# Optimization experiments

Measured on AMD Instinct MI355X. Metric: run time of the kernel, lower is better.

Reference implementation:

```python
import jax, jax.numpy as jnp
import numpy as np

N_B, N_A = 32, 48
H_IN, E_IN, H_H, H_G, NCELLS = 64, 32, 64, 16, 5


def setup_inputs() -> dict:
    key = jax.random.key(0)
    ks = jax.random.split(key, 10)
    A = (jax.random.uniform(ks[0], (N_B, N_A, N_A)) < 0.3).astype(jnp.float32)
    h = jax.random.normal(ks[1], (N_B, N_A, H_IN), dtype=jnp.float32)
    E = jax.random.normal(ks[2], (N_B, N_A, N_A, E_IN), dtype=jnp.float32)
    s_h = 1.0 / np.sqrt(H_IN)
    s_e = 1.0 / np.sqrt(E_IN)
    s_g = 1.0 / np.sqrt(H_H)
    W_h = jax.random.uniform(ks[3], (H_IN, H_H), minval=-s_h, maxval=s_h)
    b_h = jax.random.uniform(ks[4], (H_H,), minval=-s_h, maxval=s_h)
    W_e = jax.random.uniform(ks[5], (E_IN, H_G * H_H), minval=-s_e, maxval=s_e)
    b_e = jax.random.uniform(ks[6], (H_G * H_H,), minval=-s_e, maxval=s_e)
    W_ih = jax.random.uniform(ks[7], (3 * H_H, H_G), minval=-s_g, maxval=s_g)
    W_hh = jax.random.uniform(ks[8], (3 * H_H, H_H), minval=-s_g, maxval=s_g)
    b_ih = jax.random.uniform(jax.random.fold_in(key, 11), (3 * H_H,), minval=-s_g, maxval=s_g)
    b_hh = jax.random.uniform(jax.random.fold_in(key, 12), (3 * H_H,), minval=-s_g, maxval=s_g)
    return {"A": A, "h": h, "E": E, "W_h": W_h, "b_h": b_h, "W_e": W_e, "b_e": b_e,
            "W_ih": W_ih, "b_ih": b_ih, "W_hh": W_hh, "b_hh": b_hh}


def _gru_cell(x, hprev, W_ih, b_ih, W_hh, b_hh):
    # PyTorch GRUCell semantics
    gi = x @ W_ih.T + b_ih      # [N, 3*H_H]
    gh = hprev @ W_hh.T + b_hh  # [N, 3*H_H]
    i_r, i_z, i_n = jnp.split(gi, 3, axis=-1)
    h_r, h_z, h_n = jnp.split(gh, 3, axis=-1)
    r = jax.nn.sigmoid(i_r + h_r)
    z = jax.nn.sigmoid(i_z + h_z)
    n = jnp.tanh(i_n + r * h_n)
    return (1.0 - z) * n + z * hprev


def reference(A, h, E, W_h, b_h, W_e, b_e, W_ih, b_ih, W_hh, b_hh):
    N_b, n_a = h.shape[0], A.shape[1]
    maskh = (jnp.sum(A, axis=-1, keepdims=True) > 0.1).astype(jnp.float32)  # [B,n,1]
    hv = jax.nn.relu(h @ W_h + b_h) * maskh                                 # [B,n,H_H]
    Ee = jax.nn.relu(E @ W_e + b_e).reshape(N_b, n_a, n_a, H_G, H_H)
    Ee = Ee * A[..., None, None]                                            # mask edges
    # E.matmul(h).sum(dim=1) == (sum_i E[b,i,j]) @ h[b,j]; precompute the i-sum
    Esum = Ee.sum(axis=1)                                                   # [B,j,G,H]
    hc = hv  # [B,n,H_H]
    for _ in range(NCELLS):
        M = jnp.einsum('bjgh,bjh->bjg', Esum, hc).reshape(N_b * n_a, H_G)
        hc = _gru_cell(M, hc.reshape(N_b * n_a, H_H), W_ih, b_ih, W_hh, b_hh)
        hc = hc.reshape(N_b, n_a, H_H)
    return hc
```

## Files before the change

### kernel.cpp

```cpp
#include <hip/hip_runtime.h>
#include <stdint.h>

#define NB 32
#define NA 48
#define HIN 64
#define EIN 32
#define HH 64
#define HG 16
#define NCELLS 5
#define GH 1024
#define EROW 40

typedef __attribute__((ext_vector_type(8))) short short8;
typedef __attribute__((ext_vector_type(4))) float float4v;

__device__ __forceinline__ unsigned short f2bf(float f) {
    union { float f; unsigned int u; } v; v.f = f;
    unsigned int u = v.u + 0x7FFF + ((v.u >> 16) & 1);
    return (unsigned short)(u >> 16);
}
__device__ __forceinline__ float bf2f(unsigned short s) {
    union { unsigned int u; float f; } v; v.u = ((unsigned int)s) << 16;
    return v.f;
}

__global__ __launch_bounds__(256) void swizzle_We(const float* __restrict__ W_e,
                                                  unsigned short* __restrict__ hiB,
                                                  unsigned short* __restrict__ loB) {
    const int o  = blockIdx.x * 256 + threadIdx.x;
    const int ct = o >> 9;
    const int l  = (o >> 3) & 63;
    const int jj = o & 7;
    const int k  = (l >> 4) * 8 + jj;
    const int c  = ct * 16 + (l & 15);
    const float x = W_e[k * GH + c];
    const unsigned short hb = f2bf(x);
    hiB[o] = hb;
    loB[o] = f2bf(x - bf2f(hb));
}

__global__ __launch_bounds__(256) void prep_gw(const float* __restrict__ W_ih,
                                               const float* __restrict__ W_hh,
                                               float4* __restrict__ gw4) {
    const int idx = blockIdx.x * 256 + threadIdx.x;
    if (idx >= 20 * 192) return;
    const int j = idx / 192;
    const int c = idx - j * 192;
    float4 v;
    if (j < 4)  v = *(const float4*)(W_ih + c * HG + 4 * j);
    else        v = *(const float4*)(W_hh + c * HH + 4 * (j - 4));
    gw4[idx] = v;
}

template <int NT>
__device__ __forceinline__ void edge_phase(
    const unsigned short* __restrict__ hiB, const unsigned short* __restrict__ loB,
    const float* __restrict__ b_e,
    const unsigned short* EcolH, const unsigned short* EcolL,
    const int* ilist, int cnt, int wave, int lane, int mrow, int quad,
    float* Esum_s)
{
    const float4v zero4 = {0.0f, 0.0f, 0.0f, 0.0f};
    short8 aH[NT ? NT : 1], aL[NT ? NT : 1];
    float4v mk[NT ? NT : 1];
    #pragma unroll
    for (int rt = 0; rt < NT; ++rt) {
        const int i = ilist[16 * rt + mrow];
        aH[rt] = *(const short8*)(&EcolH[i * EROW + quad * 8]);
        aL[rt] = *(const short8*)(&EcolL[i * EROW + quad * 8]);
        #pragma unroll
        for (int rg = 0; rg < 4; ++rg)
            mk[rt][rg] = (16 * rt + quad * 4 + rg < cnt) ? 1.0f : 0.0f;
    }
    #pragma unroll 4
    for (int t = 0; t < 16; ++t) {
        const int ct = wave * 16 + t;
        const short8 bfH = *(const short8*)(hiB + (size_t)ct * 512 + lane * 8);
        const short8 bfL = *(const short8*)(loB + (size_t)ct * 512 + lane * 8);
        const float be = b_e[ct * 16 + mrow];
        float psum = 0.0f;
        #pragma unroll
        for (int rt = 0; rt < NT; ++rt) {
            float4v d = __builtin_amdgcn_mfma_f32_16x16x32_bf16(aL[rt], bfH, zero4, 0, 0, 0);
            d = __builtin_amdgcn_mfma_f32_16x16x32_bf16(aH[rt], bfL, d, 0, 0, 0);
            d = __builtin_amdgcn_mfma_f32_16x16x32_bf16(aH[rt], bfH, d, 0, 0, 0);
            #pragma unroll
            for (int rg = 0; rg < 4; ++rg)
                psum = fmaf(fmaxf(d[rg] + be, 0.0f), mk[rt][rg], psum);
        }
        psum += __shfl_xor(psum, 16);
        psum += __shfl_xor(psum, 32);
        if (lane < 16) {
            const int c = ct * 16 + lane;
            Esum_s[(c >> 6) * 68 + (c & 63)] = psum;
        }
    }
}

__global__ __launch_bounds__(256, 4) void fused_kernel(
    const float* __restrict__ A,  const float* __restrict__ h,
    const float* __restrict__ E,
    const float* __restrict__ W_h, const float* __restrict__ b_h,
    const float* __restrict__ b_e,
    const float* __restrict__ b_ih, const float* __restrict__ b_hh,
    const unsigned short* __restrict__ hiB, const unsigned short* __restrict__ loB,
    const float4* __restrict__ gw4,
    float* __restrict__ out)
{
    __shared__ unsigned short EcolH[NA * EROW];
    __shared__ unsigned short EcolL[NA * EROW];
    __shared__ float Esum_s[16 * 68];
    __shared__ int   ilist[NA];
    __shared__ int   cnt_s;
    __shared__ float hc_s[HH];
    __shared__ float M_s[HG];
    __shared__ float gsum_s[2 * HH];
    __shared__ float gin_s[HH], ghn_s[HH];

    const int node = blockIdx.x;
    const int b = node / NA, j = node - b * NA;
    const int tid = threadIdx.x, lane = tid & 63, wave = tid >> 6;
    const int mrow = lane & 15, quad = lane >> 4;

    for (int idx = tid; idx < NA * 8; idx += 256) {
        const int r = idx >> 3, q = idx & 7;
        const float4 ev = *(const float4*)(E + ((size_t)(b * NA + r) * NA + j) * EIN + 4 * q);
        unsigned short h0 = f2bf(ev.x), h1 = f2bf(ev.y), h2 = f2bf(ev.z), h3 = f2bf(ev.w);
        unsigned short l0 = f2bf(ev.x - bf2f(h0)), l1 = f2bf(ev.y - bf2f(h1));
        unsigned short l2 = f2bf(ev.z - bf2f(h2)), l3 = f2bf(ev.w - bf2f(h3));
        *(uint2*)(&EcolH[r * EROW + 4 * q]) =
            make_uint2((unsigned int)h0 | ((unsigned int)h1 << 16),
                       (unsigned int)h2 | ((unsigned int)h3 << 16));
        *(uint2*)(&EcolL[r * EROW + 4 * q]) =
            make_uint2((unsigned int)l0 | ((unsigned int)l1 << 16),
                       (unsigned int)l2 | ((unsigned int)l3 << 16));
    }
    if (tid < 64) {
        if (tid < NA) ilist[tid] = 0;
        const float a = (tid < NA) ? A[((size_t)b * NA + tid) * NA + j] : 0.0f;
        const unsigned long long m = __ballot(a != 0.0f);
        if (a != 0.0f) ilist[__popcll(m & ((1ull << tid) - 1ull))] = tid;
        if (tid == 0) cnt_s = (int)__popcll(m);
    }
    __syncthreads();

    const int cnt = cnt_s;
    if (cnt == 0)
        edge_phase<0>(hiB, loB, b_e, EcolH, EcolL, ilist, cnt, wave, lane, mrow, quad, Esum_s);
    else if (cnt <= 16)
        edge_phase<1>(hiB, loB, b_e, EcolH, EcolL, ilist, cnt, wave, lane, mrow, quad, Esum_s);
    else if (cnt <= 32)
        edge_phase<2>(hiB, loB, b_e, EcolH, EcolL, ilist, cnt, wave, lane, mrow, quad, Esum_s);
    else
        edge_phase<3>(hiB, loB, b_e, EcolH, EcolL, ilist, cnt, wave, lane, mrow, quad, Esum_s);

    float bihc = 0.0f, bhhc = 0.0f;
    if (tid < 3 * HH) { bihc = b_ih[tid]; bhhc = b_hh[tid]; }

    if (tid < HH) {
        const float a = (lane < NA) ? A[(size_t)node * NA + lane] : 0.0f;
        const unsigned long long mrowm = __ballot(a != 0.0f);
        const float maskh = (mrowm != 0ull) ? 1.0f : 0.0f;
        const float hr = h[(size_t)node * HIN + lane];
        float acc = b_h[lane];
        #pragma unroll
        for (int k = 0; k < HIN; ++k)
            acc = fmaf(__shfl(hr, k), W_h[k * HH + lane], acc);
        hc_s[lane] = fmaxf(acc, 0.0f) * maskh;
    }
    __syncthreads();

    #pragma unroll 1
    for (int it = 0; it < NCELLS; ++it) {
        {
            const int g = tid >> 4, q = tid & 15;
            const float4v e4 = *(const float4v*)(Esum_s + g * 68 + 4 * q);
            const float4v h4 = *(const float4v*)(hc_s + 4 * q);
            float p = e4[0] * h4[0];
            p = fmaf(e4[1], h4[1], p);
            p = fmaf(e4[2], h4[2], p);
            p = fmaf(e4[3], h4[3], p);
            p += __shfl_xor(p, 1);
            p += __shfl_xor(p, 2);
            p += __shfl_xor(p, 4);
            p += __shfl_xor(p, 8);
            if (q == 0) M_s[g] = p;
        }
        __syncthreads();
        if (tid < 3 * HH) {
            const float4* gp = gw4 + tid;
            float gi0 = bihc, gi1 = 0.0f;
            #pragma unroll
            for (int jj = 0; jj < 4; jj += 2) {
                const float4 w0 = gp[jj * 192];
                const float4 w1 = gp[(jj + 1) * 192];
                const float4v m0 = *(const float4v*)(M_s + 4 * jj);
                const float4v m1 = *(const float4v*)(M_s + 4 * jj + 4);
                gi0 = fmaf(m0[0], w0.x, gi0); gi1 = fmaf(m0[1], w0.y, gi1);
                gi0 = fmaf(m0[2], w0.z, gi0); gi1 = fmaf(m0[3], w0.w, gi1);
                gi0 = fmaf(m1[0], w1.x, gi0); gi1 = fmaf(m1[1], w1.y, gi1);
                gi0 = fmaf(m1[2], w1.z, gi0); gi1 = fmaf(m1[3], w1.w, gi1);
            }
            float gh0 = bhhc, gh1 = 0.0f, gh2 = 0.0f, gh3 = 0.0f;
            #pragma unroll
            for (int jj = 4; jj < 20; jj += 2) {
                const float4 w0 = gp[jj * 192];
                const float4 w1 = gp[(jj + 1) * 192];
                const float4v h0 = *(const float4v*)(hc_s + 4 * (jj - 4));
                const float4v h1 = *(const float4v*)(hc_s + 4 * (jj - 4) + 4);
                gh0 = fmaf(h0[0], w0.x, gh0); gh1 = fmaf(h0[1], w0.y, gh1);
                gh2 = fmaf(h0[2], w0.z, gh2); gh3 = fmaf(h0[3], w0.w, gh3);
                gh0 = fmaf(h1[0], w1.x, gh0); gh1 = fmaf(h1[1], w1.y, gh1);
                gh2 = fmaf(h1[2], w1.z, gh2); gh3 = fmaf(h1[3], w1.w, gh3);
            }
            const float gi = gi0 + gi1;
            const float gh = (gh0 + gh1) + (gh2 + gh3);
            if (tid < 2 * HH) gsum_s[tid] = gi + gh;
            else { gin_s[tid - 2 * HH] = gi; ghn_s[tid - 2 * HH] = gh; }
        }
        __syncthreads();
        if (tid < HH) {
            const float r = 1.0f / (1.0f + __expf(-gsum_s[tid]));
            const float z = 1.0f / (1.0f + __expf(-gsum_s[HH + tid]));
            const float nin = gin_s[tid] + r * ghn_s[tid];
            const float n = 1.0f - 2.0f / (__expf(2.0f * nin) + 1.0f);
            hc_s[tid] = (1.0f - z) * n + z * hc_s[tid];
        }
        __syncthreads();
    }

    if (tid < HH) out[(size_t)node * HH + tid] = hc_s[tid];
}

extern "C" void kernel_launch(void* const* d_in, const int* in_sizes, int n_in,
                              void* d_out, int out_size, void* d_ws, size_t ws_size,
                              hipStream_t stream) {
    const float* A    = (const float*)d_in[0];
    const float* h    = (const float*)d_in[1];
    const float* E    = (const float*)d_in[2];
    const float* W_h  = (const float*)d_in[3];
    const float* b_h  = (const float*)d_in[4];
    const float* W_e  = (const float*)d_in[5];
    const float* b_e  = (const float*)d_in[6];
    const float* W_ih = (const float*)d_in[7];
    const float* b_ih = (const float*)d_in[8];
    const float* W_hh = (const float*)d_in[9];
    const float* b_hh = (const float*)d_in[10];
    unsigned short* hiB = (unsigned short*)d_ws;
    unsigned short* loB = hiB + 32768;
    float4* gw4 = (float4*)(loB + 32768);
    float* out = (float*)d_out;

    hipLaunchKernelGGL(swizzle_We, dim3(128), dim3(256), 0, stream, W_e, hiB, loB);
    hipLaunchKernelGGL(prep_gw, dim3(15), dim3(256), 0, stream, W_ih, W_hh, gw4);
    hipLaunchKernelGGL(fused_kernel, dim3(NB * NA), dim3(256), 0, stream,
                       A, h, E, W_h, b_h, b_e, b_ih, b_hh, hiB, loB, gw4, out);
}
```

Measured before the change: 121.1 us.

## Process three nodes per block to reuse W_e and GRU weight loads

Each block now handles three destination nodes instead of one, so every W_e hi/lo fragment and every GRU weight float4 loaded from global memory is reused across three nodes' MFMA and FMA work. The gather of E rows is compacted by adjacency list, and the edge tile count is set by the largest count among the three nodes. This cuts global weight traffic and block count by a factor of three. In exchange it raises register and LDS use, drops the occupancy hint from 4 to 2 blocks, and does extra MFMA work for nodes with fewer edges than the maximum.

New measurement: 113.4 us. 1.07x faster.

```diff
diff --git a/kernel.cpp b/kernel.cpp
--- a/kernel.cpp
+++ b/kernel.cpp
@@ -10,6 +10,8 @@
 #define NCELLS 5
 #define GH 1024
 #define EROW 40
+#define P3 3
+#define ESTR 1088
 
 typedef __attribute__((ext_vector_type(8))) short short8;
 typedef __attribute__((ext_vector_type(4))) float float4v;
@@ -52,52 +54,60 @@
     gw4[idx] = v;
 }
 
-template <int NT>
-__device__ __forceinline__ void edge_phase(
+template <int NTMAX>
+__device__ __forceinline__ void edge_phase3(
     const unsigned short* __restrict__ hiB, const unsigned short* __restrict__ loB,
     const float* __restrict__ b_e,
     const unsigned short* EcolH, const unsigned short* EcolL,
-    const int* ilist, int cnt, int wave, int lane, int mrow, int quad,
+    const float* mask_s,
+    int wave, int lane, int mrow, int quad,
     float* Esum_s)
 {
     const float4v zero4 = {0.0f, 0.0f, 0.0f, 0.0f};
-    short8 aH[NT ? NT : 1], aL[NT ? NT : 1];
-    float4v mk[NT ? NT : 1];
+    short8 aH[P3][NTMAX ? NTMAX : 1], aL[P3][NTMAX ? NTMAX : 1];
     #pragma unroll
-    for (int rt = 0; rt < NT; ++rt) {
-        const int i = ilist[16 * rt + mrow];
-        aH[rt] = *(const short8*)(&EcolH[i * EROW + quad * 8]);
-        aL[rt] = *(const short8*)(&EcolL[i * EROW + quad * 8]);
+    for (int p = 0; p < P3; ++p)
         #pragma unroll
-        for (int rg = 0; rg < 4; ++rg)
-            mk[rt][rg] = (16 * rt + quad * 4 + rg < cnt) ? 1.0f : 0.0f;
-    }
-    #pragma unroll 4
+        for (int rt = 0; rt < NTMAX; ++rt) {
+            const int off = (p * 48 + 16 * rt + mrow) * EROW + quad * 8;
+            aH[p][rt] = *(const short8*)(EcolH + off);
+            aL[p][rt] = *(const short8*)(EcolL + off);
+        }
+
+    #pragma unroll 2
     for (int t = 0; t < 16; ++t) {
         const int ct = wave * 16 + t;
         const short8 bfH = *(const short8*)(hiB + (size_t)ct * 512 + lane * 8);
         const short8 bfL = *(const short8*)(loB + (size_t)ct * 512 + lane * 8);
         const float be = b_e[ct * 16 + mrow];
-        float psum = 0.0f;
+        float psum[P3] = {0.0f, 0.0f, 0.0f};
         #pragma unroll
-        for (int rt = 0; rt < NT; ++rt) {
-            float4v d = __builtin_amdgcn_mfma_f32_16x16x32_bf16(aL[rt], bfH, zero4, 0, 0, 0);
-            d = __builtin_amdgcn_mfma_f32_16x16x32_bf16(aH[rt], bfL, d, 0, 0, 0);
-            d = __builtin_amdgcn_mfma_f32_16x16x32_bf16(aH[rt], bfH, d, 0, 0, 0);
+        for (int p = 0; p < P3; ++p) {
             #pragma unroll
-            for (int rg = 0; rg < 4; ++rg)
-                psum = fmaf(fmaxf(d[rg] + be, 0.0f), mk[rt][rg], psum);
-        }
-        psum += __shfl_xor(psum, 16);
-        psum += __shfl_xor(psum, 32);
-        if (lane < 16) {
-            const int c = ct * 16 + lane;
-            Esum_s[(c >> 6) * 68 + (c & 63)] = psum;
-        }
-    }
-}
-
-__global__ __launch_bounds__(256, 4) void fused_kernel(
+            for (int rt = 0; rt < NTMAX; ++rt) {
+                float4v d = __builtin_amdgcn_mfma_f32_16x16x32_bf16(aL[p][rt], bfH, zero4, 0, 0, 0);
+                d = __builtin_amdgcn_mfma_f32_16x16x32_bf16(aH[p][rt], bfL, d, 0, 0, 0);
+                d = __builtin_amdgcn_mfma_f32_16x16x32_bf16(aH[p][rt], bfH, d, 0, 0, 0);
+                const float4v mk = *(const float4v*)(mask_s + p * 48 + rt * 16 + quad * 4);
+                #pragma unroll
+                for (int rg = 0; rg < 4; ++rg)
+                    psum[p] = fmaf(fmaxf(d[rg] + be, 0.0f), mk[rg], psum[p]);
+            }
+        }
+        #pragma unroll
+        for (int p = 0; p < P3; ++p) {
+            float ps = psum[p];
+            ps += __shfl_xor(ps, 16);
+            ps += __shfl_xor(ps, 32);
+            if (lane < 16) {
+                const int c = ct * 16 + lane;
+                Esum_s[p * ESTR + (c >> 6) * 68 + (c & 63)] = ps;
+            }
+        }
+    }
+}
+
+__global__ __launch_bounds__(256, 2) void fused_kernel(
     const float* __restrict__ A,  const float* __restrict__ h,
     const float* __restrict__ E,
     const float* __restrict__ W_h, const float* __restrict__ b_h,
@@ -107,57 +117,72 @@
     const float4* __restrict__ gw4,
     float* __restrict__ out)
 {
-    __shared__ unsigned short EcolH[NA * EROW];
-    __shared__ unsigned short EcolL[NA * EROW];
-    __shared__ float Esum_s[16 * 68];
-    __shared__ int   ilist[NA];
-    __shared__ int   cnt_s;
-    __shared__ float hc_s[HH];
-    __shared__ float M_s[HG];
-    __shared__ float gsum_s[2 * HH];
-    __shared__ float gin_s[HH], ghn_s[HH];
-
-    const int node = blockIdx.x;
-    const int b = node / NA, j = node - b * NA;
+    __shared__ unsigned short EcolH[P3 * NA * EROW];
+    __shared__ unsigned short EcolL[P3 * NA * EROW];
+    __shared__ float Esum_s[P3 * ESTR];
+    __shared__ float mask_s[P3 * 48];
+    __shared__ int   ilist[P3 * NA];
+    __shared__ int   cnt_s[P3];
+    __shared__ float hc_s[P3 * HH];
+    __shared__ float M_s[P3 * HG];
+    __shared__ float gsum_s[P3 * 2 * HH];
+    __shared__ float gin_s[P3 * HH], ghn_s[P3 * HH];
+
+    const int node0 = blockIdx.x * P3;
+    const int b = node0 / NA, j0 = node0 - b * NA;
     const int tid = threadIdx.x, lane = tid & 63, wave = tid >> 6;
     const int mrow = lane & 15, quad = lane >> 4;
 
-    for (int idx = tid; idx < NA * 8; idx += 256) {
-        const int r = idx >> 3, q = idx & 7;
-        const float4 ev = *(const float4*)(E + ((size_t)(b * NA + r) * NA + j) * EIN + 4 * q);
-        unsigned short h0 = f2bf(ev.x), h1 = f2bf(ev.y), h2 = f2bf(ev.z), h3 = f2bf(ev.w);
-        unsigned short l0 = f2bf(ev.x - bf2f(h0)), l1 = f2bf(ev.y - bf2f(h1));
-        unsigned short l2 = f2bf(ev.z - bf2f(h2)), l3 = f2bf(ev.w - bf2f(h3));
-        *(uint2*)(&EcolH[r * EROW + 4 * q]) =
-            make_uint2((unsigned int)h0 | ((unsigned int)h1 << 16),
-                       (unsigned int)h2 | ((unsigned int)h3 << 16));
-        *(uint2*)(&EcolL[r * EROW + 4 * q]) =
-            make_uint2((unsigned int)l0 | ((unsigned int)l1 << 16),
-                       (unsigned int)l2 | ((unsigned int)l3 << 16));
-    }
-    if (tid < 64) {
-        if (tid < NA) ilist[tid] = 0;
-        const float a = (tid < NA) ? A[((size_t)b * NA + tid) * NA + j] : 0.0f;
+    if (wave < P3) {
+        const float a = (lane < NA) ? A[((size_t)b * NA + lane) * NA + (j0 + wave)] : 0.0f;
         const unsigned long long m = __ballot(a != 0.0f);
-        if (a != 0.0f) ilist[__popcll(m & ((1ull << tid) - 1ull))] = tid;
-        if (tid == 0) cnt_s = (int)__popcll(m);
+        if (a != 0.0f) ilist[wave * NA + __popcll(m & ((1ull << lane) - 1ull))] = lane;
+        if (lane == 0) cnt_s[wave] = (int)__popcll(m);
     }
     __syncthreads();
 
-    const int cnt = cnt_s;
-    if (cnt == 0)
-        edge_phase<0>(hiB, loB, b_e, EcolH, EcolL, ilist, cnt, wave, lane, mrow, quad, Esum_s);
-    else if (cnt <= 16)
-        edge_phase<1>(hiB, loB, b_e, EcolH, EcolL, ilist, cnt, wave, lane, mrow, quad, Esum_s);
-    else if (cnt <= 32)
-        edge_phase<2>(hiB, loB, b_e, EcolH, EcolL, ilist, cnt, wave, lane, mrow, quad, Esum_s);
+    for (int idx = tid; idx < P3 * NA * 8; idx += 256) {
+        const int p = idx / (NA * 8);
+        const int rem = idx - p * (NA * 8);
+        const int r = rem >> 3, q = rem & 7;
+        uint2 hv2 = make_uint2(0u, 0u), lv2 = make_uint2(0u, 0u);
+        if (r < cnt_s[p]) {
+            const int i = ilist[p * NA + r];
+            const float4 ev = *(const float4*)(E + ((size_t)(b * NA + i) * NA + (j0 + p)) * EIN + 4 * q);
+            unsigned short h0 = f2bf(ev.x), h1 = f2bf(ev.y), h2 = f2bf(ev.z), h3 = f2bf(ev.w);
+            unsigned short l0 = f2bf(ev.x - bf2f(h0)), l1 = f2bf(ev.y - bf2f(h1));
+            unsigned short l2 = f2bf(ev.z - bf2f(h2)), l3 = f2bf(ev.w - bf2f(h3));
+            hv2 = make_uint2((unsigned int)h0 | ((unsigned int)h1 << 16),
+                             (unsigned int)h2 | ((unsigned int)h3 << 16));
+            lv2 = make_uint2((unsigned int)l0 | ((unsigned int)l1 << 16),
+                             (unsigned int)l2 | ((unsigned int)l3 << 16));
+        }
+        *(uint2*)(&EcolH[(p * NA + r) * EROW + 4 * q]) = hv2;
+        *(uint2*)(&EcolL[(p * NA + r) * EROW + 4 * q]) = lv2;
+    }
+    if (tid < P3 * 48) {
+        const int p = tid / 48, rem = tid - p * 48;
+        mask_s[tid] = (rem < cnt_s[p]) ? 1.0f : 0.0f;
+    }
+    __syncthreads();
+
+    const int nt0 = (cnt_s[0] + 15) >> 4, nt1 = (cnt_s[1] + 15) >> 4, nt2 = (cnt_s[2] + 15) >> 4;
+    int ntmax = nt0 > nt1 ? nt0 : nt1; ntmax = ntmax > nt2 ? ntmax : nt2;
+
+    if (ntmax == 0)
+        edge_phase3<0>(hiB, loB, b_e, EcolH, EcolL, mask_s, wave, lane, mrow, quad, Esum_s);
+    else if (ntmax == 1)
+        edge_phase3<1>(hiB, loB, b_e, EcolH, EcolL, mask_s, wave, lane, mrow, quad, Esum_s);
+    else if (ntmax == 2)
+        edge_phase3<2>(hiB, loB, b_e, EcolH, EcolL, mask_s, wave, lane, mrow, quad, Esum_s);
     else
-        edge_phase<3>(hiB, loB, b_e, EcolH, EcolL, ilist, cnt, wave, lane, mrow, quad, Esum_s);
+        edge_phase3<3>(hiB, loB, b_e, EcolH, EcolL, mask_s, wave, lane, mrow, quad, Esum_s);
 
     float bihc = 0.0f, bhhc = 0.0f;
     if (tid < 3 * HH) { bihc = b_ih[tid]; bhhc = b_hh[tid]; }
 
-    if (tid < HH) {
+    if (wave < P3) {
+        const int node = node0 + wave;
         const float a = (lane < NA) ? A[(size_t)node * NA + lane] : 0.0f;
         const unsigned long long mrowm = __ballot(a != 0.0f);
         const float maskh = (mrowm != 0ull) ? 1.0f : 0.0f;
@@ -166,70 +191,87 @@
         #pragma unroll
         for (int k = 0; k < HIN; ++k)
             acc = fmaf(__shfl(hr, k), W_h[k * HH + lane], acc);
-        hc_s[lane] = fmaxf(acc, 0.0f) * maskh;
+        hc_s[wave * HH + lane] = fmaxf(acc, 0.0f) * maskh;
     }
     __syncthreads();
 
     #pragma unroll 1
     for (int it = 0; it < NCELLS; ++it) {
-        {
-            const int g = tid >> 4, q = tid & 15;
-            const float4v e4 = *(const float4v*)(Esum_s + g * 68 + 4 * q);
-            const float4v h4 = *(const float4v*)(hc_s + 4 * q);
-            float p = e4[0] * h4[0];
-            p = fmaf(e4[1], h4[1], p);
-            p = fmaf(e4[2], h4[2], p);
-            p = fmaf(e4[3], h4[3], p);
-            p += __shfl_xor(p, 1);
-            p += __shfl_xor(p, 2);
-            p += __shfl_xor(p, 4);
-            p += __shfl_xor(p, 8);
-            if (q == 0) M_s[g] = p;
+        if (tid < 192) {
+            const int p = tid >> 6, s = tid & 63, g = s >> 2, q = s & 3;
+            const float* ep = Esum_s + p * ESTR + g * 68 + q * 16;
+            const float* hp = hc_s + p * HH + q * 16;
+            const float4v e0 = *(const float4v*)(ep),     h0 = *(const float4v*)(hp);
+            const float4v e1 = *(const float4v*)(ep + 4), h1 = *(const float4v*)(hp + 4);
+            const float4v e2 = *(const float4v*)(ep + 8), h2 = *(const float4v*)(hp + 8);
+            const float4v e3 = *(const float4v*)(ep + 12), h3 = *(const float4v*)(hp + 12);
+            float pp = e0[0] * h0[0];
+            pp = fmaf(e0[1], h0[1], pp); pp = fmaf(e0[2], h0[2], pp); pp = fmaf(e0[3], h0[3], pp);
+            pp = fmaf(e1[0], h1[0], pp); pp = fmaf(e1[1], h1[1], pp);
+            pp = fmaf(e1[2], h1[2], pp); pp = fmaf(e1[3], h1[3], pp);
+            pp = fmaf(e2[0], h2[0], pp); pp = fmaf(e2[1], h2[1], pp);
+            pp = fmaf(e2[2], h2[2], pp); pp = fmaf(e2[3], h2[3], pp);
+            pp = fmaf(e3[0], h3[0], pp); pp = fmaf(e3[1], h3[1], pp);
+            pp = fmaf(e3[2], h3[2], pp); pp = fmaf(e3[3], h3[3], pp);
+            pp += __shfl_xor(pp, 1);
+            pp += __shfl_xor(pp, 2);
+            if (q == 0) M_s[p * HG + g] = pp;
         }
         __syncthreads();
-        if (tid < 3 * HH) {
+        if (tid < 192) {
             const float4* gp = gw4 + tid;
-            float gi0 = bihc, gi1 = 0.0f;
+            float gi0 = bihc, gi1 = bihc, gi2 = bihc;
             #pragma unroll
-            for (int jj = 0; jj < 4; jj += 2) {
-                const float4 w0 = gp[jj * 192];
-                const float4 w1 = gp[(jj + 1) * 192];
-                const float4v m0 = *(const float4v*)(M_s + 4 * jj);
-                const float4v m1 = *(const float4v*)(M_s + 4 * jj + 4);
-                gi0 = fmaf(m0[0], w0.x, gi0); gi1 = fmaf(m0[1], w0.y, gi1);
-                gi0 = fmaf(m0[2], w0.z, gi0); gi1 = fmaf(m0[3], w0.w, gi1);
-                gi0 = fmaf(m1[0], w1.x, gi0); gi1 = fmaf(m1[1], w1.y, gi1);
-                gi0 = fmaf(m1[2], w1.z, gi0); gi1 = fmaf(m1[3], w1.w, gi1);
-            }
-            float gh0 = bhhc, gh1 = 0.0f, gh2 = 0.0f, gh3 = 0.0f;
+            for (int jj = 0; jj < 4; ++jj) {
+                const float4 w = gp[jj * 192];
+                const float4v m0 = *(const float4v*)(M_s + 0 * HG + 4 * jj);
+                const float4v m1 = *(const float4v*)(M_s + 1 * HG + 4 * jj);
+                const float4v m2 = *(const float4v*)(M_s + 2 * HG + 4 * jj);
+                gi0 = fmaf(m0[0], w.x, gi0); gi0 = fmaf(m0[1], w.y, gi0);
+                gi0 = fmaf(m0[2], w.z, gi0); gi0 = fmaf(m0[3], w.w, gi0);
+                gi1 = fmaf(m1[0], w.x, gi1); gi1 = fmaf(m1[1], w.y, gi1);
+                gi1 = fmaf(m1[2], w.z, gi1); gi1 = fmaf(m1[3], w.w, gi1);
+                gi2 = fmaf(m2[0], w.x, gi2); gi2 = fmaf(m2[1], w.y, gi2);
+                gi2 = fmaf(m2[2], w.z, gi2); gi2 = fmaf(m2[3], w.w, gi2);
+            }
+            float gh0 = bhhc, gh1 = bhhc, gh2 = bhhc;
             #pragma unroll
-            for (int jj = 4; jj < 20; jj += 2) {
-                const float4 w0 = gp[jj * 192];
-                const float4 w1 = gp[(jj + 1) * 192];
-                const float4v h0 = *(const float4v*)(hc_s + 4 * (jj - 4));
-                const float4v h1 = *(const float4v*)(hc_s + 4 * (jj - 4) + 4);
-                gh0 = fmaf(h0[0], w0.x, gh0); gh1 = fmaf(h0[1], w0.y, gh1);
-                gh2 = fmaf(h0[2], w0.z, gh2); gh3 = fmaf(h0[3], w0.w, gh3);
-                gh0 = fmaf(h1[0], w1.x, gh0); gh1 = fmaf(h1[1], w1.y, gh1);
-                gh2 = fmaf(h1[2], w1.z, gh2); gh3 = fmaf(h1[3], w1.w, gh3);
-            }
-            const float gi = gi0 + gi1;
-            const float gh = (gh0 + gh1) + (gh2 + gh3);
-            if (tid < 2 * HH) gsum_s[tid] = gi + gh;
-            else { gin_s[tid - 2 * HH] = gi; ghn_s[tid - 2 * HH] = gh; }
+            for (int jj = 4; jj < 20; ++jj) {
+                const float4 w = gp[jj * 192];
+                const float4v h0 = *(const float4v*)(hc_s + 0 * HH + 4 * (jj - 4));
+                const float4v h1 = *(const float4v*)(hc_s + 1 * HH + 4 * (jj - 4));
+                const float4v h2 = *(const float4v*)(hc_s + 2 * HH + 4 * (jj - 4));
+                gh0 = fmaf(h0[0], w.x, gh0); gh0 = fmaf(h0[1], w.y, gh0);
+                gh0 = fmaf(h0[2], w.z, gh0); gh0 = fmaf(h0[3], w.w, gh0);
+                gh1 = fmaf(h1[0], w.x, gh1); gh1 = fmaf(h1[1], w.y, gh1);
+                gh1 = fmaf(h1[2], w.z, gh1); gh1 = fmaf(h1[3], w.w, gh1);
+                gh2 = fmaf(h2[0], w.x, gh2); gh2 = fmaf(h2[1], w.y, gh2);
+                gh2 = fmaf(h2[2], w.z, gh2); gh2 = fmaf(h2[3], w.w, gh2);
+            }
+            if (tid < 2 * HH) {
+                gsum_s[0 * 2 * HH + tid] = gi0 + gh0;
+                gsum_s[1 * 2 * HH + tid] = gi1 + gh1;
+                gsum_s[2 * 2 * HH + tid] = gi2 + gh2;
+            } else {
+                const int c = tid - 2 * HH;
+                gin_s[0 * HH + c] = gi0; ghn_s[0 * HH + c] = gh0;
+                gin_s[1 * HH + c] = gi1; ghn_s[1 * HH + c] = gh1;
+                gin_s[2 * HH + c] = gi2; ghn_s[2 * HH + c] = gh2;
+            }
         }
         __syncthreads();
-        if (tid < HH) {
-            const float r = 1.0f / (1.0f + __expf(-gsum_s[tid]));
-            const float z = 1.0f / (1.0f + __expf(-gsum_s[HH + tid]));
-            const float nin = gin_s[tid] + r * ghn_s[tid];
+        if (tid < 192) {
+            const int p = tid >> 6, c = tid & 63;
+            const float r = 1.0f / (1.0f + __expf(-gsum_s[p * 2 * HH + c]));
+            const float z = 1.0f / (1.0f + __expf(-gsum_s[p * 2 * HH + HH + c]));
+            const float nin = gin_s[p * HH + c] + r * ghn_s[p * HH + c];
             const float n = 1.0f - 2.0f / (__expf(2.0f * nin) + 1.0f);
-            hc_s[tid] = (1.0f - z) * n + z * hc_s[tid];
+            hc_s[p * HH + c] = (1.0f - z) * n + z * hc_s[p * HH + c];
         }
         __syncthreads();
     }
 
-    if (tid < HH) out[(size_t)node * HH + tid] = hc_s[tid];
+    if (tid < 192) out[(size_t)node0 * HH + tid] = hc_s[tid];
 }
 
 extern "C" void kernel_launch(void* const* d_in, const int* in_sizes, int n_in,
@@ -253,6 +295,6 @@
 
     hipLaunchKernelGGL(swizzle_We, dim3(128), dim3(256), 0, stream, W_e, hiB, loB);
     hipLaunchKernelGGL(prep_gw, dim3(15), dim3(256), 0, stream, W_ih, W_hh, gw4);
-    hipLaunchKernelGGL(fused_kernel, dim3(NB * NA), dim3(256), 0, stream,
+    hipLaunchKernelGGL(fused_kernel, dim3(NB * NA / P3), dim3(256), 0, stream,
                        A, h, E, W_h, b_h, b_e, b_ih, b_hh, hiB, loB, gw4, out);
 }
```
